# Kernel tuning notes

Measured on AMD Instinct MI355X. Metric: run time of the kernel, lower is better.

The kernel has to match this reference:

```python
import jax, jax.numpy as jnp
import numpy as np

EMBED_DIM = 256
FFN_DIM = 512


def layer_norm_2d(x, gamma, beta, eps=1e-5):
    # GroupNorm(num_groups=1): normalize over (C,H,W) per sample, per-channel affine.
    mean = jnp.mean(x, axis=(1, 2, 3), keepdims=True)
    var = jnp.var(x, axis=(1, 2, 3), keepdims=True)
    xh = (x - mean) * jax.lax.rsqrt(var + eps)
    return xh * gamma[None, :, None, None] + beta[None, :, None, None]


def conv1x1(x, W, b):
    # W: [out_ch, in_ch]; x: [B, C, H, W]
    return jnp.einsum('oc,bchw->bohw', W, x) + b[None, :, None, None]


def sep_attn(x, Wqkv, bqkv, Wout, bout):
    C = EMBED_DIM
    qkv = conv1x1(x, Wqkv, bqkv)                       # [B, 1+2C, H, W]
    q = qkv[:, :1]                                     # [B, 1, H, W]
    k = qkv[:, 1:1 + C]                                # [B, C, H, W]
    v = qkv[:, 1 + C:]                                 # [B, C, H, W]
    scores = jax.nn.softmax(q, axis=-1)                # softmax over last dim
    ctx = jnp.sum(k * scores, axis=-1, keepdims=True)  # [B, C, H, 1]
    out = jax.nn.relu(v) * ctx                         # broadcast over last dim
    return conv1x1(out, Wout, bout)


def setup_inputs() -> dict:
    key = jax.random.key(0)
    ks = jax.random.split(key, 20)
    C, F = EMBED_DIM, FFN_DIM
    B, P, N = 16, 64, 256
    s = 1.0 / np.sqrt(C)
    inp = {
        'x': jax.random.normal(ks[0], (B, C, P, N), jnp.float32),
        # attn branch 1 (transposed)
        'g1': jnp.ones((C,), jnp.float32),
        'b1': jnp.zeros((C,), jnp.float32),
        'Wqkv1': jax.random.normal(ks[1], (1 + 2 * C, C), jnp.float32) * s,
        'bqkv1': jnp.zeros((1 + 2 * C,), jnp.float32),
        'Wout1': jax.random.normal(ks[2], (C, C), jnp.float32) * s,
        'bout1': jnp.zeros((C,), jnp.float32),
        # attn branch 2
        'g2': jnp.ones((C,), jnp.float32),
        'b2': jnp.zeros((C,), jnp.float32),
        'Wqkv2': jax.random.normal(ks[3], (1 + 2 * C, C), jnp.float32) * s,
        'bqkv2': jnp.zeros((1 + 2 * C,), jnp.float32),
        'Wout2': jax.random.normal(ks[4], (C, C), jnp.float32) * s,
        'bout2': jnp.zeros((C,), jnp.float32),
        # FFN
        'gf': jnp.ones((C,), jnp.float32),
        'bf': jnp.zeros((C,), jnp.float32),
        'Wf1': jax.random.normal(ks[5], (F, C), jnp.float32) * s,
        'bf1': jnp.zeros((F,), jnp.float32),
        'Wf2': jax.random.normal(ks[6], (C, F), jnp.float32) * (1.0 / np.sqrt(F)),
        'bf2': jnp.zeros((C,), jnp.float32),
    }
    return inp


def reference(x, g1, b1, Wqkv1, bqkv1, Wout1, bout1,
              g2, b2, Wqkv2, bqkv2, Wout2, bout2,
              gf, bf, Wf1, bf1, Wf2, bf2):
    res = x
    # branch 1: attend over dim 2 (patch axis) via transpose of last two dims
    xp = jnp.swapaxes(x, 2, 3)
    xp = sep_attn(layer_norm_2d(xp, g1, b1), Wqkv1, bqkv1, Wout1, bout1)
    xp = jnp.swapaxes(xp, 2, 3)
    # branch 2: attend over last dim
    x2 = sep_attn(layer_norm_2d(x, g2, b2), Wqkv2, bqkv2, Wout2, bout2)
    x = x2 + xp + res
    # pre-norm conv FFN with Hardtanh
    h = conv1x1(layer_norm_2d(x, gf, bf), Wf1, bf1)
    h = jnp.clip(h, -1.0, 1.0)
    x = x + conv1x1(h, Wf2, bf2)
    return x
```

## Files before the change

kernel.cpp:

```cpp
#include <hip/hip_runtime.h>

typedef __bf16 bf16x8 __attribute__((ext_vector_type(8)));
typedef float floatx4 __attribute__((ext_vector_type(4)));
typedef unsigned short u16;

#define MFMA16(A,Bv,Cv) __builtin_amdgcn_mfma_f32_16x16x32_bf16(A,Bv,Cv,0,0,0)

__device__ __forceinline__ u16 f2bf(float f){
  unsigned u = __float_as_uint(f);
  return (u16)((u + 0x7fffu + ((u >> 16) & 1u)) >> 16);
}

#define LDK 264
#define LDO 520

__global__ void k_prep(const float* __restrict__ Wqkv1, const float* __restrict__ g1, const float* __restrict__ b1,
                       const float* __restrict__ Wqkv2, const float* __restrict__ g2, const float* __restrict__ b2,
                       const float* __restrict__ Wout1, const float* __restrict__ Wout2,
                       const float* __restrict__ Wf1, const float* __restrict__ gf, const float* __restrict__ bfv,
                       const float* __restrict__ Wf2, const float* __restrict__ bout1, const float* __restrict__ bout2,
                       float* __restrict__ Wk1g, float* __restrict__ Wk2g,
                       u16* __restrict__ Wv1g, u16* __restrict__ Wv2g, u16* __restrict__ Wo1, u16* __restrict__ Wo2,
                       u16* __restrict__ Wf1g, u16* __restrict__ Wf2b,
                       float* __restrict__ Ak1, float* __restrict__ Bk1, float* __restrict__ Av1, float* __restrict__ Bv1,
                       float* __restrict__ Ak2, float* __restrict__ Bk2, float* __restrict__ Av2, float* __restrict__ Bv2,
                       float* __restrict__ A3, float* __restrict__ B3, float* __restrict__ bsum)
{
  int bid = blockIdx.x, c = threadIdx.x;
  __shared__ float sa[4], sb[4];
  int wv = c >> 6, ln = c & 63;
  auto rowsum2 = [&](float a, float bb, float* pA, float* pB){
    for(int off=32; off; off>>=1){ a += __shfl_down(a,off,64); bb += __shfl_down(bb,off,64); }
    if(ln==0){ sa[wv]=a; sb[wv]=bb; }
    __syncthreads();
    if(c==0){ *pA = sa[0]+sa[1]+sa[2]+sa[3]; *pB = sb[0]+sb[1]+sb[2]+sb[3]; }
  };
  if(bid < 512){
    int r = bid; float w = Wqkv1[(size_t)(1+r)*256 + c];
    if(r < 256){ float wg = w*g1[c]; Wk1g[(size_t)r*256+c] = wg; rowsum2(wg, w*b1[c], &Ak1[r], &Bk1[r]); }
    else { int rv=r-256; float wg=w*g1[c]; Wv1g[(size_t)rv*256+c] = f2bf(wg); rowsum2(wg, w*b1[c], &Av1[rv], &Bv1[rv]); }
  } else if(bid < 1024){
    int r = bid-512; float w = Wqkv2[(size_t)(1+r)*256 + c];
    if(r < 256){ float wg = w*g2[c]; Wk2g[(size_t)r*256+c] = wg; rowsum2(wg, w*b2[c], &Ak2[r], &Bk2[r]); }
    else { int rv=r-256; float wg=w*g2[c]; Wv2g[(size_t)rv*256+c] = f2bf(wg); rowsum2(wg, w*b2[c], &Av2[rv], &Bv2[rv]); }
  } else if(bid < 1280){
    int r = bid-1024; Wo1[(size_t)r*256+c] = f2bf(Wout1[(size_t)r*256+c]);
    if(bid==1024) bsum[c] = bout1[c] + bout2[c];
  } else if(bid < 1536){
    int r = bid-1280; Wo2[(size_t)r*256+c] = f2bf(Wout2[(size_t)r*256+c]);
  } else if(bid < 2048){
    int r = bid-1536; float w = Wf1[(size_t)r*256+c]; float wg = w*gf[c];
    Wf1g[(size_t)r*256+c] = f2bf(wg); rowsum2(wg, w*bfv[c], &A3[r], &B3[r]);
  } else {
    int r = bid-2048;
    Wf2b[(size_t)r*512+c]     = f2bf(Wf2[(size_t)r*512+c]);
    Wf2b[(size_t)r*512+256+c] = f2bf(Wf2[(size_t)r*512+256+c]);
  }
}

__global__ void k_stats_q(const float* __restrict__ x,
                          const float* __restrict__ Wqkv1, const float* __restrict__ g1,
                          const float* __restrict__ Wqkv2, const float* __restrict__ g2,
                          float* __restrict__ stats,
                          float* __restrict__ rawq1, float* __restrict__ rawq2)
{
  int bid = blockIdx.x; int b = bid >> 6, p = bid & 63;
  int n = threadIdx.x;
  __shared__ float wq1[256], wq2[256];
  __shared__ float sred[4], ssred[4];
  wq1[n] = Wqkv1[n]*g1[n];
  wq2[n] = Wqkv2[n]*g2[n];
  __syncthreads();
  const float* xp = x + ((size_t)b*4194304 + (size_t)p*256 + n);
  float s=0.f, ss=0.f, q1=0.f, q2=0.f;
  #pragma unroll 4
  for(int c=0;c<256;c++){
    float v = xp[(size_t)c*16384];
    s += v; ss += v*v; q1 += wq1[c]*v; q2 += wq2[c]*v;
  }
  rawq2[(size_t)bid*256 + n] = q2;
  rawq1[((size_t)(b*256 + n))*64 + p] = q1;
  int wv = n>>6, ln = n&63;
  for(int off=32; off; off>>=1){ s += __shfl_down(s,off,64); ss += __shfl_down(ss,off,64); }
  if(ln==0){ sred[wv]=s; ssred[wv]=ss; }
  __syncthreads();
  if(n==0){
    atomicAdd(&stats[b],    sred[0]+sred[1]+sred[2]+sred[3]);
    atomicAdd(&stats[16+b], ssred[0]+ssred[1]+ssred[2]+ssred[3]);
  }
}

__global__ void k_finalize(const float* __restrict__ stats, float* __restrict__ derived)
{
  int b = threadIdx.x;
  if(b < 16){
    float M = 4194304.f;
    float mean = stats[b]/M;
    float var  = stats[16+b]/M - mean*mean;
    derived[b] = mean;
    derived[16+b] = rsqrtf(var + 1e-5f);
  }
}

__global__ void k_tvec(const float* __restrict__ derived,
                       const float* __restrict__ bqkv1, const float* __restrict__ bqkv2,
                       const float* __restrict__ Ak1, const float* __restrict__ Bk1,
                       const float* __restrict__ Av1, const float* __restrict__ Bv1,
                       const float* __restrict__ Ak2, const float* __restrict__ Bk2,
                       const float* __restrict__ Av2, const float* __restrict__ Bv2,
                       float* __restrict__ tk1, float* __restrict__ tv1,
                       float* __restrict__ tk2, float* __restrict__ tv2)
{
  int b = blockIdx.x, c = threadIdx.x;
  float mr = derived[b]*derived[16+b];
  tk1[b*256+c] = bqkv1[1+c]   + Bk1[c] - mr*Ak1[c];
  tv1[b*256+c] = bqkv1[257+c] + Bv1[c] - mr*Av1[c];
  tk2[b*256+c] = bqkv2[1+c]   + Bk2[c] - mr*Ak2[c];
  tv2[b*256+c] = bqkv2[257+c] + Bv2[c] - mr*Av2[c];
}

__global__ void k_softmax2(const float* __restrict__ rawq2, const float* __restrict__ derived,
                           float* __restrict__ scores2)
{
  int row = blockIdx.x; int b = row >> 6; int tid = threadIdx.x;
  __shared__ float sm[4], ssum[4];
  int wv = tid>>6, ln = tid&63;
  float v = derived[16+b]*rawq2[(size_t)row*256 + tid];
  float m = v;
  for(int off=32; off; off>>=1) m = fmaxf(m, __shfl_xor(m,off,64));
  if(ln==0) sm[wv]=m;
  __syncthreads();
  m = fmaxf(fmaxf(sm[0],sm[1]),fmaxf(sm[2],sm[3]));
  float e = __expf(v-m);
  float s = e;
  for(int off=32; off; off>>=1) s += __shfl_xor(s,off,64);
  if(ln==0) ssum[wv]=s;
  __syncthreads();
  s = ssum[0]+ssum[1]+ssum[2]+ssum[3];
  scores2[(size_t)row*256 + tid] = e/s;
}

__global__ void k_softmax1(const float* __restrict__ rawq1, const float* __restrict__ derived,
                           float* __restrict__ scores1)
{
  int row = blockIdx.x; int b = row >> 8; int tid = threadIdx.x;
  float v = derived[16+b]*rawq1[(size_t)row*64 + tid];
  float m = v;
  for(int off=32; off; off>>=1) m = fmaxf(m, __shfl_xor(m,off,64));
  float e = __expf(v-m);
  float s = e;
  for(int off=32; off; off>>=1) s += __shfl_xor(s,off,64);
  scores1[(size_t)row*64 + tid] = e/s;
}

__global__ void k_xs(const float* __restrict__ x,
                     const float* __restrict__ scores1, const float* __restrict__ scores2,
                     float* __restrict__ xs1, float* __restrict__ xs2)
{
  __shared__ float X[64*257];
  __shared__ float part[256];
  int bid = blockIdx.x; int b = bid >> 8, c = bid & 255;
  int tid = threadIdx.x;
  const float* xp = x + ((size_t)b*4194304 + (size_t)c*16384);
  for(int i=tid; i<16384; i+=256){
    int p = i >> 8, n = i & 255;
    X[p*257 + n] = xp[i];
  }
  __syncthreads();
  {
    int n = tid;
    const float* s1 = scores1 + (size_t)(b*256 + n)*64;
    float acc = 0.f;
    #pragma unroll 8
    for(int p=0;p<64;p++) acc += s1[p]*X[p*257+n];
    xs1[(size_t)(b*256 + c)*256 + n] = acc;
  }
  {
    int p = tid & 63, q = tid >> 6;
    const float* s2 = scores2 + (size_t)(b*64 + p)*256;
    float acc = 0.f;
    #pragma unroll 8
    for(int i=0;i<64;i++){ int n = q*64 + i; acc += s2[n]*X[p*257+n]; }
    part[tid] = acc;
    __syncthreads();
    if(q==0)
      xs2[(size_t)(b*256 + c)*64 + p] = part[p] + part[64+p] + part[128+p] + part[192+p];
  }
}

__global__ void k_ctx2(const float* __restrict__ Wk2g, const float* __restrict__ xs2,
                       const float* __restrict__ tk2, const float* __restrict__ derived,
                       float* __restrict__ ctx2)
{
  __shared__ float xv[4][256];
  int bid = blockIdx.x; int b = bid >> 4, pg = (bid & 15) << 2;
  int o = threadIdx.x;
  #pragma unroll
  for(int j=0;j<4;j++) xv[j][o] = xs2[(size_t)(b*256 + o)*64 + pg + j];
  __syncthreads();
  const float* w = Wk2g + (size_t)o*256;
  float a0=0,a1=0,a2=0,a3=0;
  for(int cc=0;cc<256;cc++){
    float wc = w[cc];
    a0 += wc*xv[0][cc]; a1 += wc*xv[1][cc]; a2 += wc*xv[2][cc]; a3 += wc*xv[3][cc];
  }
  float r = derived[16+b], t = tk2[b*256 + o];
  ctx2[(size_t)(b*64 + pg+0)*256 + o] = r*a0 + t;
  ctx2[(size_t)(b*64 + pg+1)*256 + o] = r*a1 + t;
  ctx2[(size_t)(b*64 + pg+2)*256 + o] = r*a2 + t;
  ctx2[(size_t)(b*64 + pg+3)*256 + o] = r*a3 + t;
}

__global__ void k_ctx1(const float* __restrict__ Wk1g, const float* __restrict__ xs1,
                       const float* __restrict__ tk1, const float* __restrict__ derived,
                       float* __restrict__ ctx1)
{
  __shared__ float xv[4][256];
  int bid = blockIdx.x; int b = bid >> 6, ng = (bid & 63) << 2;
  int o = threadIdx.x;
  #pragma unroll
  for(int j=0;j<4;j++) xv[j][o] = xs1[(size_t)(b*256 + o)*256 + ng + j];
  __syncthreads();
  const float* w = Wk1g + (size_t)o*256;
  float a0=0,a1=0,a2=0,a3=0;
  for(int cc=0;cc<256;cc++){
    float wc = w[cc];
    a0 += wc*xv[0][cc]; a1 += wc*xv[1][cc]; a2 += wc*xv[2][cc]; a3 += wc*xv[3][cc];
  }
  float r = derived[16+b], t = tk1[b*256 + o];
  ctx1[(size_t)(b*256 + ng+0)*256 + o] = r*a0 + t;
  ctx1[(size_t)(b*256 + ng+1)*256 + o] = r*a1 + t;
  ctx1[(size_t)(b*256 + ng+2)*256 + o] = r*a2 + t;
  ctx1[(size_t)(b*256 + ng+3)*256 + o] = r*a3 + t;
}

__global__ __launch_bounds__(256,2) void k_attn(
    const float* __restrict__ x,
    const u16* __restrict__ Wv1g, const u16* __restrict__ Wv2g,
    const u16* __restrict__ Wo1, const u16* __restrict__ Wo2,
    const float* __restrict__ tv1, const float* __restrict__ tv2,
    const float* __restrict__ ctx1, const float* __restrict__ ctx2,
    const float* __restrict__ bsum, const float* __restrict__ derived,
    float* __restrict__ out, float* __restrict__ stats)
{
  __shared__ u16 Xs[64*LDK];
  __shared__ u16 Os[64*LDK];
  __shared__ float rs[4], rss[4];
  int bid = blockIdx.x;
  int b = bid >> 8, p = (bid >> 2) & 63, n0 = (bid & 3) << 6;
  int tid = threadIdx.x, wv = tid >> 6, lane = tid & 63, lr = lane & 15, lq = lane >> 4;
  float rstd = derived[16+b];

  {
    int pix = tid & 63, c0 = (tid >> 6) * 2;
    const float* xp = x + ((size_t)b*4194304 + (size_t)p*256 + n0 + pix);
    for(int cc = c0; cc < 256; cc += 8){
      float v0 = xp[(size_t)cc*16384];
      float v1 = xp[(size_t)(cc+1)*16384];
      unsigned pk = (unsigned)f2bf(rstd*v0) | ((unsigned)f2bf(rstd*v1) << 16);
      *(unsigned*)&Xs[pix*LDK + cc] = pk;
    }
  }
  __syncthreads();

  floatx4 Dv[4][4], Dy[4][4];
  #pragma unroll
  for(int i=0;i<4;i++){
    #pragma unroll
    for(int j=0;j<4;j++) Dy[i][j] = floatx4{0.f,0.f,0.f,0.f};
  }

  auto gemmX = [&](const u16* __restrict__ W){
    #pragma unroll
    for(int i=0;i<4;i++){
      #pragma unroll
      for(int j=0;j<4;j++) Dv[i][j] = floatx4{0.f,0.f,0.f,0.f};
    }
    for(int k0=0;k0<256;k0+=32){
      bf16x8 Bf[4];
      #pragma unroll
      for(int pt=0;pt<4;pt++) Bf[pt] = *(const bf16x8*)&Xs[(pt*16+lr)*LDK + k0 + lq*8];
      #pragma unroll
      for(int ct=0;ct<4;ct++){
        bf16x8 Af = *(const bf16x8*)&W[(size_t)(wv*64+ct*16+lr)*256 + k0 + lq*8];
        #pragma unroll
        for(int pt=0;pt<4;pt++) Dv[ct][pt] = MFMA16(Af, Bf[pt], Dv[ct][pt]);
      }
    }
  };
  auto gemmO = [&](const u16* __restrict__ W){
    for(int k0=0;k0<256;k0+=32){
      bf16x8 Bf[4];
      #pragma unroll
      for(int pt=0;pt<4;pt++) Bf[pt] = *(const bf16x8*)&Os[(pt*16+lr)*LDK + k0 + lq*8];
      #pragma unroll
      for(int ct=0;ct<4;ct++){
        bf16x8 Af = *(const bf16x8*)&W[(size_t)(wv*64+ct*16+lr)*256 + k0 + lq*8];
        #pragma unroll
        for(int pt=0;pt<4;pt++) Dy[ct][pt] = MFMA16(Af, Bf[pt], Dy[ct][pt]);
      }
    }
  };

  gemmX(Wv2g);
  {
    const float* c2row = ctx2 + (size_t)(b*64+p)*256;
    #pragma unroll
    for(int ct=0;ct<4;ct++){
      int cbase = wv*64 + ct*16 + lq*4;
      float4 tvv = *(const float4*)&tv2[b*256 + cbase];
      float4 cx  = *(const float4*)&c2row[cbase];
      float tb[4] = {tvv.x,tvv.y,tvv.z,tvv.w};
      float cb[4] = {cx.x,cx.y,cx.z,cx.w};
      #pragma unroll
      for(int pt=0;pt<4;pt++){
        int pix = pt*16 + lr;
        unsigned lo = (unsigned)f2bf(fmaxf(Dv[ct][pt][0]+tb[0],0.f)*cb[0])
                    | ((unsigned)f2bf(fmaxf(Dv[ct][pt][1]+tb[1],0.f)*cb[1]) << 16);
        unsigned hi = (unsigned)f2bf(fmaxf(Dv[ct][pt][2]+tb[2],0.f)*cb[2])
                    | ((unsigned)f2bf(fmaxf(Dv[ct][pt][3]+tb[3],0.f)*cb[3]) << 16);
        uint2 o4; o4.x=lo; o4.y=hi;
        *(uint2*)&Os[pix*LDK + cbase] = o4;
      }
    }
  }
  __syncthreads();
  gemmO(Wo2);
  __syncthreads();

  gemmX(Wv1g);
  {
    #pragma unroll
    for(int ct=0;ct<4;ct++){
      int cbase = wv*64 + ct*16 + lq*4;
      float4 tvv = *(const float4*)&tv1[b*256 + cbase];
      float tb[4] = {tvv.x,tvv.y,tvv.z,tvv.w};
      #pragma unroll
      for(int pt=0;pt<4;pt++){
        int pix = pt*16 + lr;
        int n = n0 + pix;
        float4 cx = *(const float4*)&ctx1[(size_t)(b*256+n)*256 + cbase];
        float cb[4] = {cx.x,cx.y,cx.z,cx.w};
        unsigned lo = (unsigned)f2bf(fmaxf(Dv[ct][pt][0]+tb[0],0.f)*cb[0])
                    | ((unsigned)f2bf(fmaxf(Dv[ct][pt][1]+tb[1],0.f)*cb[1]) << 16);
        unsigned hi = (unsigned)f2bf(fmaxf(Dv[ct][pt][2]+tb[2],0.f)*cb[2])
                    | ((unsigned)f2bf(fmaxf(Dv[ct][pt][3]+tb[3],0.f)*cb[3]) << 16);
        uint2 o4; o4.x=lo; o4.y=hi;
        *(uint2*)&Os[pix*LDK + cbase] = o4;
      }
    }
  }
  __syncthreads();
  gemmO(Wo1);

  float s3=0.f, ss3=0.f;
  #pragma unroll
  for(int ct=0;ct<4;ct++){
    int cbase = wv*64 + ct*16 + lq*4;
    float4 bsv = *(const float4*)&bsum[cbase];
    float bb[4] = {bsv.x,bsv.y,bsv.z,bsv.w};
    #pragma unroll
    for(int pt=0;pt<4;pt++){
      int pix = pt*16 + lr;
      size_t base = (size_t)b*4194304 + (size_t)cbase*16384 + (size_t)p*256 + n0 + pix;
      #pragma unroll
      for(int r=0;r<4;r++){
        size_t a = base + (size_t)r*16384;
        float v = Dy[ct][pt][r] + bb[r] + x[a];
        out[a] = v;
        s3 += v; ss3 += v*v;
      }
    }
  }
  for(int off=32; off; off>>=1){ s3 += __shfl_down(s3,off,64); ss3 += __shfl_down(ss3,off,64); }
  if(lane==0){ rs[wv]=s3; rss[wv]=ss3; }
  __syncthreads();
  if(tid==0){
    atomicAdd(&stats[32+b], rs[0]+rs[1]+rs[2]+rs[3]);
    atomicAdd(&stats[48+b], rss[0]+rss[1]+rss[2]+rss[3]);
  }
}

__global__ void k_finalize3(const float* __restrict__ stats, float* __restrict__ derived,
                            const float* __restrict__ bf1, const float* __restrict__ A3,
                            const float* __restrict__ B3, float* __restrict__ t3)
{
  int tid = threadIdx.x;
  if(tid < 16){
    float M = 4194304.f;
    float mean = stats[32+tid]/M;
    float var  = stats[48+tid]/M - mean*mean;
    derived[32+tid] = mean;
    derived[48+tid] = rsqrtf(var + 1e-5f);
  }
  __syncthreads();
  float a = A3[tid], bb = B3[tid], bias = bf1[tid];
  for(int b=0;b<16;b++){
    float mr = derived[32+b]*derived[48+b];
    t3[b*512 + tid] = bias + bb - mr*a;
  }
}

__global__ __launch_bounds__(256,2) void k_ffn(
    const u16* __restrict__ Wf1g, const u16* __restrict__ Wf2b,
    const float* __restrict__ t3, const float* __restrict__ bf2,
    const float* __restrict__ derived,
    float* __restrict__ out)
{
  __shared__ u16 Xs[32*LDK];
  __shared__ u16 Os[32*LDO];
  int bid = blockIdx.x;
  int b = bid >> 9, p = (bid >> 3) & 63, n0 = (bid & 7) << 5;
  int tid = threadIdx.x, wv = tid >> 6, lane = tid & 63, lr = lane & 15, lq = lane >> 4;
  float rstd = derived[48+b];

  {
    int pix = tid & 31, c0 = (tid >> 5) * 2;
    const float* xp = out + ((size_t)b*4194304 + (size_t)p*256 + n0 + pix);
    for(int cc = c0; cc < 256; cc += 16){
      float v0 = xp[(size_t)cc*16384];
      float v1 = xp[(size_t)(cc+1)*16384];
      unsigned pk = (unsigned)f2bf(rstd*v0) | ((unsigned)f2bf(rstd*v1) << 16);
      *(unsigned*)&Xs[pix*LDK + cc] = pk;
    }
  }
  __syncthreads();

  floatx4 Dh[8][2];
  #pragma unroll
  for(int i=0;i<8;i++){ Dh[i][0] = floatx4{0.f,0.f,0.f,0.f}; Dh[i][1] = floatx4{0.f,0.f,0.f,0.f}; }
  for(int k0=0;k0<256;k0+=32){
    bf16x8 Bf[2];
    #pragma unroll
    for(int pt=0;pt<2;pt++) Bf[pt] = *(const bf16x8*)&Xs[(pt*16+lr)*LDK + k0 + lq*8];
    #pragma unroll
    for(int ct=0;ct<8;ct++){
      bf16x8 Af = *(const bf16x8*)&Wf1g[(size_t)(wv*128+ct*16+lr)*256 + k0 + lq*8];
      Dh[ct][0] = MFMA16(Af, Bf[0], Dh[ct][0]);
      Dh[ct][1] = MFMA16(Af, Bf[1], Dh[ct][1]);
    }
  }
  #pragma unroll
  for(int ct=0;ct<8;ct++){
    int fbase = wv*128 + ct*16 + lq*4;
    float4 tt = *(const float4*)&t3[b*512 + fbase];
    float tb[4] = {tt.x,tt.y,tt.z,tt.w};
    #pragma unroll
    for(int pt=0;pt<2;pt++){
      int pix = pt*16 + lr;
      unsigned lo = (unsigned)f2bf(fminf(fmaxf(Dh[ct][pt][0]+tb[0],-1.f),1.f))
                  | ((unsigned)f2bf(fminf(fmaxf(Dh[ct][pt][1]+tb[1],-1.f),1.f)) << 16);
      unsigned hi = (unsigned)f2bf(fminf(fmaxf(Dh[ct][pt][2]+tb[2],-1.f),1.f))
                  | ((unsigned)f2bf(fminf(fmaxf(Dh[ct][pt][3]+tb[3],-1.f),1.f)) << 16);
      uint2 o4; o4.x=lo; o4.y=hi;
      *(uint2*)&Os[pix*LDO + fbase] = o4;
    }
  }
  __syncthreads();

  floatx4 Dy[4][2];
  #pragma unroll
  for(int i=0;i<4;i++){ Dy[i][0] = floatx4{0.f,0.f,0.f,0.f}; Dy[i][1] = floatx4{0.f,0.f,0.f,0.f}; }
  for(int k0=0;k0<512;k0+=32){
    bf16x8 Bf[2];
    #pragma unroll
    for(int pt=0;pt<2;pt++) Bf[pt] = *(const bf16x8*)&Os[(pt*16+lr)*LDO + k0 + lq*8];
    #pragma unroll
    for(int ct=0;ct<4;ct++){
      bf16x8 Af = *(const bf16x8*)&Wf2b[(size_t)(wv*64+ct*16+lr)*512 + k0 + lq*8];
      Dy[ct][0] = MFMA16(Af, Bf[0], Dy[ct][0]);
      Dy[ct][1] = MFMA16(Af, Bf[1], Dy[ct][1]);
    }
  }

  #pragma unroll
  for(int ct=0;ct<4;ct++){
    int obase = wv*64 + ct*16 + lq*4;
    float4 bbv = *(const float4*)&bf2[obase];
    float bb[4] = {bbv.x,bbv.y,bbv.z,bbv.w};
    #pragma unroll
    for(int pt=0;pt<2;pt++){
      int pix = pt*16 + lr;
      size_t base = (size_t)b*4194304 + (size_t)obase*16384 + (size_t)p*256 + n0 + pix;
      #pragma unroll
      for(int r=0;r<4;r++){
        size_t a = base + (size_t)r*16384;
        out[a] = out[a] + Dy[ct][pt][r] + bb[r];
      }
    }
  }
}

extern "C" void kernel_launch(void* const* d_in, const int* in_sizes, int n_in,
                              void* d_out, int out_size, void* d_ws, size_t ws_size,
                              hipStream_t stream)
{
  const float* x     = (const float*)d_in[0];
  const float* g1    = (const float*)d_in[1];
  const float* b1    = (const float*)d_in[2];
  const float* Wqkv1 = (const float*)d_in[3];
  const float* bqkv1 = (const float*)d_in[4];
  const float* Wout1 = (const float*)d_in[5];
  const float* bout1 = (const float*)d_in[6];
  const float* g2    = (const float*)d_in[7];
  const float* b2    = (const float*)d_in[8];
  const float* Wqkv2 = (const float*)d_in[9];
  const float* bqkv2 = (const float*)d_in[10];
  const float* Wout2 = (const float*)d_in[11];
  const float* bout2 = (const float*)d_in[12];
  const float* gf    = (const float*)d_in[13];
  const float* bfv   = (const float*)d_in[14];
  const float* Wf1   = (const float*)d_in[15];
  const float* bf1   = (const float*)d_in[16];
  const float* Wf2   = (const float*)d_in[17];
  const float* bf2   = (const float*)d_in[18];
  float* out = (float*)d_out;
  char* ws = (char*)d_ws;

  float* stats   = (float*)(ws + 0);
  float* derived = (float*)(ws + 256);
  float* bsum    = (float*)(ws + 512);
  float* Ak1 = (float*)(ws + 1536);
  float* Bk1 = (float*)(ws + 2560);
  float* Av1 = (float*)(ws + 3584);
  float* Bv1 = (float*)(ws + 4608);
  float* Ak2 = (float*)(ws + 5632);
  float* Bk2 = (float*)(ws + 6656);
  float* Av2 = (float*)(ws + 7680);
  float* Bv2 = (float*)(ws + 8704);
  float* A3  = (float*)(ws + 9728);
  float* B3  = (float*)(ws + 11776);
  float* tk1 = (float*)(ws + 13824);
  float* tv1 = (float*)(ws + 30208);
  float* tk2 = (float*)(ws + 46592);
  float* tv2 = (float*)(ws + 62976);
  float* t3  = (float*)(ws + 79360);
  float* Wk1g = (float*)(ws + 112128);
  float* Wk2g = (float*)(ws + 374272);
  u16* Wv1g = (u16*)(ws + 636416);
  u16* Wv2g = (u16*)(ws + 767488);
  u16* Wo1  = (u16*)(ws + 898560);
  u16* Wo2  = (u16*)(ws + 1029632);
  u16* Wf1g = (u16*)(ws + 1160704);
  u16* Wf2b = (u16*)(ws + 1422848);
  float* rawq1   = (float*)(ws + 1684992);
  float* rawq2   = (float*)(ws + 2733568);
  float* scores1 = (float*)(ws + 3782144);
  float* scores2 = (float*)(ws + 4830720);
  float* xs1  = (float*)(ws + 5879296);
  float* xs2  = (float*)(ws + 10073600);
  float* ctx1 = (float*)(ws + 11122176);
  float* ctx2 = (float*)(ws + 15316480);

  hipMemsetAsync(stats, 0, 64*sizeof(float), stream);

  k_prep<<<2304, 256, 0, stream>>>(Wqkv1,g1,b1, Wqkv2,g2,b2, Wout1,Wout2, Wf1,gf,bfv, Wf2, bout1,bout2,
                                   Wk1g,Wk2g, Wv1g,Wv2g,Wo1,Wo2,Wf1g,Wf2b,
                                   Ak1,Bk1,Av1,Bv1, Ak2,Bk2,Av2,Bv2, A3,B3, bsum);
  k_stats_q<<<1024, 256, 0, stream>>>(x, Wqkv1,g1, Wqkv2,g2, stats, rawq1, rawq2);
  k_finalize<<<1, 64, 0, stream>>>(stats, derived);
  k_tvec<<<16, 256, 0, stream>>>(derived, bqkv1,bqkv2, Ak1,Bk1,Av1,Bv1, Ak2,Bk2,Av2,Bv2,
                                 tk1,tv1,tk2,tv2);
  k_softmax2<<<1024, 256, 0, stream>>>(rawq2, derived, scores2);
  k_softmax1<<<4096, 64, 0, stream>>>(rawq1, derived, scores1);
  k_xs<<<4096, 256, 0, stream>>>(x, scores1, scores2, xs1, xs2);
  k_ctx2<<<256, 256, 0, stream>>>(Wk2g, xs2, tk2, derived, ctx2);
  k_ctx1<<<1024, 256, 0, stream>>>(Wk1g, xs1, tk1, derived, ctx1);
  k_attn<<<4096, 256, 0, stream>>>(x, Wv1g,Wv2g, Wo1,Wo2, tv1,tv2, ctx1,ctx2,
                                   bsum, derived, out, stats);
  k_finalize3<<<1, 512, 0, stream>>>(stats, derived, bf1, A3, B3, t3);
  k_ffn<<<8192, 256, 0, stream>>>(Wf1g, Wf2b, t3, bf2, derived, out);
}
```

Baseline: 1.662 ms.

## Emit channel-last bf16 copy of residual in attn and add fast FFN reading it

The attention kernel now also writes a bf16, pixel-major, channel-contiguous copy of the post-attention activations into workspace. A new FFN kernel reads its MFMA B operands straight from that copy instead of re-reading and converting the fp32 output through shared memory, which frees LDS and allows higher occupancy. The stats/q kernel is also changed to load four pixels per thread as vectors with fewer blocks. This adds an extra bf16 write of the activations and only takes the fast path when the workspace is large enough; otherwise it falls back to the old FFN kernel.

```diff
diff --git a/kernel.cpp b/kernel.cpp
--- a/kernel.cpp
+++ b/kernel.cpp
@@ -64,27 +64,34 @@
                           float* __restrict__ stats,
                           float* __restrict__ rawq1, float* __restrict__ rawq2)
 {
-  int bid = blockIdx.x; int b = bid >> 6, p = bid & 63;
-  int n = threadIdx.x;
+  int bid = blockIdx.x; int b = bid >> 4, chunk = bid & 15;
+  int tid = threadIdx.x;
   __shared__ float wq1[256], wq2[256];
   __shared__ float sred[4], ssred[4];
-  wq1[n] = Wqkv1[n]*g1[n];
-  wq2[n] = Wqkv2[n]*g2[n];
-  __syncthreads();
-  const float* xp = x + ((size_t)b*4194304 + (size_t)p*256 + n);
-  float s=0.f, ss=0.f, q1=0.f, q2=0.f;
+  wq1[tid] = Wqkv1[tid]*g1[tid];
+  wq2[tid] = Wqkv2[tid]*g2[tid];
+  __syncthreads();
+  int pix0 = chunk*1024 + tid*4;
+  int p = pix0 >> 8, n = pix0 & 255;
+  const float* xp = x + ((size_t)b << 22) + pix0;
+  float s = 0.f, ss = 0.f;
+  floatx4 q1 = {0.f,0.f,0.f,0.f}, q2 = {0.f,0.f,0.f,0.f};
   #pragma unroll 4
   for(int c=0;c<256;c++){
-    float v = xp[(size_t)c*16384];
-    s += v; ss += v*v; q1 += wq1[c]*v; q2 += wq2[c]*v;
-  }
-  rawq2[(size_t)bid*256 + n] = q2;
-  rawq1[((size_t)(b*256 + n))*64 + p] = q1;
-  int wv = n>>6, ln = n&63;
+    floatx4 v = *(const floatx4*)&xp[(size_t)c << 14];
+    s  += v[0]+v[1]+v[2]+v[3];
+    ss += v[0]*v[0]+v[1]*v[1]+v[2]*v[2]+v[3]*v[3];
+    q1 += wq1[c]*v;
+    q2 += wq2[c]*v;
+  }
+  *(floatx4*)&rawq2[(size_t)(b*64 + p)*256 + n] = q2;
+  #pragma unroll
+  for(int i=0;i<4;i++) rawq1[((size_t)(b*256 + n + i))*64 + p] = q1[i];
+  int wv = tid>>6, ln = tid&63;
   for(int off=32; off; off>>=1){ s += __shfl_down(s,off,64); ss += __shfl_down(ss,off,64); }
   if(ln==0){ sred[wv]=s; ssred[wv]=ss; }
   __syncthreads();
-  if(n==0){
+  if(tid==0){
     atomicAdd(&stats[b],    sred[0]+sred[1]+sred[2]+sred[3]);
     atomicAdd(&stats[16+b], ssred[0]+ssred[1]+ssred[2]+ssred[3]);
   }
@@ -241,7 +248,8 @@
     const float* __restrict__ tv1, const float* __restrict__ tv2,
     const float* __restrict__ ctx1, const float* __restrict__ ctx2,
     const float* __restrict__ bsum, const float* __restrict__ derived,
-    float* __restrict__ out, float* __restrict__ stats)
+    float* __restrict__ out, float* __restrict__ stats,
+    u16* __restrict__ xb)
 {
   __shared__ u16 Xs[64*LDK];
   __shared__ u16 Os[64*LDK];
@@ -363,12 +371,20 @@
     for(int pt=0;pt<4;pt++){
       int pix = pt*16 + lr;
       size_t base = (size_t)b*4194304 + (size_t)cbase*16384 + (size_t)p*256 + n0 + pix;
+      float vv[4];
       #pragma unroll
       for(int r=0;r<4;r++){
         size_t a = base + (size_t)r*16384;
         float v = Dy[ct][pt][r] + bb[r] + x[a];
         out[a] = v;
+        vv[r] = v;
         s3 += v; ss3 += v*v;
+      }
+      if(xb){
+        uint2 pk;
+        pk.x = (unsigned)f2bf(vv[0]) | ((unsigned)f2bf(vv[1]) << 16);
+        pk.y = (unsigned)f2bf(vv[2]) | ((unsigned)f2bf(vv[3]) << 16);
+        *(uint2*)&xb[((size_t)(b*16384 + p*256 + n0 + pix) << 8) + cbase] = pk;
       }
     }
   }
@@ -398,6 +414,86 @@
   for(int b=0;b<16;b++){
     float mr = derived[32+b]*derived[48+b];
     t3[b*512 + tid] = bias + bb - mr*a;
+  }
+}
+
+__global__ __launch_bounds__(256,4) void k_ffn_fast(
+    const u16* __restrict__ xb,
+    const u16* __restrict__ Wf1g, const u16* __restrict__ Wf2b,
+    const float* __restrict__ t3, const float* __restrict__ bf2,
+    const float* __restrict__ derived,
+    float* __restrict__ out)
+{
+  __shared__ u16 Os[32*LDO];
+  int bid = blockIdx.x;
+  int b = bid >> 9, p = (bid >> 3) & 63, n0 = (bid & 7) << 5;
+  int tid = threadIdx.x, wv = tid >> 6, lane = tid & 63, lr = lane & 15, lq = lane >> 4;
+  float rstd = derived[48+b];
+
+  const u16* xrow = xb + ((size_t)(b*16384 + p*256 + n0) << 8);
+
+  floatx4 Dh[8][2];
+  #pragma unroll
+  for(int i=0;i<8;i++){ Dh[i][0] = floatx4{0.f,0.f,0.f,0.f}; Dh[i][1] = floatx4{0.f,0.f,0.f,0.f}; }
+  for(int k0=0;k0<256;k0+=32){
+    bf16x8 Bf[2];
+    #pragma unroll
+    for(int pt=0;pt<2;pt++) Bf[pt] = *(const bf16x8*)&xrow[((size_t)(pt*16+lr) << 8) + k0 + lq*8];
+    #pragma unroll
+    for(int ct=0;ct<8;ct++){
+      bf16x8 Af = *(const bf16x8*)&Wf1g[(size_t)(wv*128+ct*16+lr)*256 + k0 + lq*8];
+      Dh[ct][0] = MFMA16(Af, Bf[0], Dh[ct][0]);
+      Dh[ct][1] = MFMA16(Af, Bf[1], Dh[ct][1]);
+    }
+  }
+  #pragma unroll
+  for(int ct=0;ct<8;ct++){
+    int fbase = wv*128 + ct*16 + lq*4;
+    float4 tt = *(const float4*)&t3[b*512 + fbase];
+    float tb[4] = {tt.x,tt.y,tt.z,tt.w};
+    #pragma unroll
+    for(int pt=0;pt<2;pt++){
+      int pix = pt*16 + lr;
+      unsigned lo = (unsigned)f2bf(fminf(fmaxf(rstd*Dh[ct][pt][0]+tb[0],-1.f),1.f))
+                  | ((unsigned)f2bf(fminf(fmaxf(rstd*Dh[ct][pt][1]+tb[1],-1.f),1.f)) << 16);
+      unsigned hi = (unsigned)f2bf(fminf(fmaxf(rstd*Dh[ct][pt][2]+tb[2],-1.f),1.f))
+                  | ((unsigned)f2bf(fminf(fmaxf(rstd*Dh[ct][pt][3]+tb[3],-1.f),1.f)) << 16);
+      uint2 o4; o4.x=lo; o4.y=hi;
+      *(uint2*)&Os[pix*LDO + fbase] = o4;
+    }
+  }
+  __syncthreads();
+
+  floatx4 Dy[4][2];
+  #pragma unroll
+  for(int i=0;i<4;i++){ Dy[i][0] = floatx4{0.f,0.f,0.f,0.f}; Dy[i][1] = floatx4{0.f,0.f,0.f,0.f}; }
+  for(int k0=0;k0<512;k0+=32){
+    bf16x8 Bf[2];
+    #pragma unroll
+    for(int pt=0;pt<2;pt++) Bf[pt] = *(const bf16x8*)&Os[(pt*16+lr)*LDO + k0 + lq*8];
+    #pragma unroll
+    for(int ct=0;ct<4;ct++){
+      bf16x8 Af = *(const bf16x8*)&Wf2b[(size_t)(wv*64+ct*16+lr)*512 + k0 + lq*8];
+      Dy[ct][0] = MFMA16(Af, Bf[0], Dy[ct][0]);
+      Dy[ct][1] = MFMA16(Af, Bf[1], Dy[ct][1]);
+    }
+  }
+
+  #pragma unroll
+  for(int ct=0;ct<4;ct++){
+    int obase = wv*64 + ct*16 + lq*4;
+    float4 bbv = *(const float4*)&bf2[obase];
+    float bb[4] = {bbv.x,bbv.y,bbv.z,bbv.w};
+    #pragma unroll
+    for(int pt=0;pt<2;pt++){
+      int pix = pt*16 + lr;
+      size_t base = (size_t)b*4194304 + (size_t)obase*16384 + (size_t)p*256 + n0 + pix;
+      #pragma unroll
+      for(int r=0;r<4;r++){
+        size_t a = base + (size_t)r*16384;
+        out[a] = out[a] + Dy[ct][pt][r] + bb[r];
+      }
+    }
   }
 }
 
@@ -551,13 +647,17 @@
   float* xs2  = (float*)(ws + 10073600);
   float* ctx1 = (float*)(ws + 11122176);
   float* ctx2 = (float*)(ws + 15316480);
+  const size_t XB_OFF  = 16777216;
+  const size_t XB_SIZE = (size_t)16*16384*256*2;
+  bool fast = (ws_size >= XB_OFF + XB_SIZE);
+  u16* xb = fast ? (u16*)(ws + XB_OFF) : (u16*)nullptr;
 
   hipMemsetAsync(stats, 0, 64*sizeof(float), stream);
 
   k_prep<<<2304, 256, 0, stream>>>(Wqkv1,g1,b1, Wqkv2,g2,b2, Wout1,Wout2, Wf1,gf,bfv, Wf2, bout1,bout2,
                                    Wk1g,Wk2g, Wv1g,Wv2g,Wo1,Wo2,Wf1g,Wf2b,
                                    Ak1,Bk1,Av1,Bv1, Ak2,Bk2,Av2,Bv2, A3,B3, bsum);
-  k_stats_q<<<1024, 256, 0, stream>>>(x, Wqkv1,g1, Wqkv2,g2, stats, rawq1, rawq2);
+  k_stats_q<<<256, 256, 0, stream>>>(x, Wqkv1,g1, Wqkv2,g2, stats, rawq1, rawq2);
   k_finalize<<<1, 64, 0, stream>>>(stats, derived);
   k_tvec<<<16, 256, 0, stream>>>(derived, bqkv1,bqkv2, Ak1,Bk1,Av1,Bv1, Ak2,Bk2,Av2,Bv2,
                                  tk1,tv1,tk2,tv2);
@@ -567,7 +667,10 @@
   k_ctx2<<<256, 256, 0, stream>>>(Wk2g, xs2, tk2, derived, ctx2);
   k_ctx1<<<1024, 256, 0, stream>>>(Wk1g, xs1, tk1, derived, ctx1);
   k_attn<<<4096, 256, 0, stream>>>(x, Wv1g,Wv2g, Wo1,Wo2, tv1,tv2, ctx1,ctx2,
-                                   bsum, derived, out, stats);
+                                   bsum, derived, out, stats, xb);
   k_finalize3<<<1, 512, 0, stream>>>(stats, derived, bf1, A3, B3, t3);
-  k_ffn<<<8192, 256, 0, stream>>>(Wf1g, Wf2b, t3, bf2, derived, out);
-}
+  if(fast)
+    k_ffn_fast<<<8192, 256, 0, stream>>>(xb, Wf1g, Wf2b, t3, bf2, derived, out);
+  else
+    k_ffn<<<8192, 256, 0, stream>>>(Wf1g, Wf2b, t3, bf2, derived, out);
+}
```

Result: no change. 1.693 ms (+1.9%).
